# Kernel optimization log

Measured on AMD Instinct MI355X. Metric: run time of the kernel, lower is better.

The kernel has to match this reference:

```python
import jax, jax.numpy as jnp
import numpy as np

DIM = 128
KS = 7
HEADS = 4
HEAD_DIM = DIM // HEADS


def setup_inputs() -> dict:
    key = jax.random.key(0)
    ks = jax.random.split(key, 10)
    B, H, W, C = 4, 64, 64, DIM
    s = 0.02
    return {
        "x": jax.random.normal(ks[0], (B, H, W, C), jnp.float32),
        "qkv_w": jax.random.normal(ks[1], (C, 3 * C), jnp.float32) * s,
        "qkv_b": jnp.zeros((3 * C,), jnp.float32),
        "proj_w": jax.random.normal(ks[2], (C, C), jnp.float32) * s,
        "proj_b": jnp.zeros((C,), jnp.float32),
        "rpb": jax.random.normal(ks[3], (HEADS, 2 * KS - 1, 2 * KS - 1), jnp.float32) * s,
        "g1_w": jax.random.normal(ks[4], (C, C // 2), jnp.float32) * s,
        "g1_b": jnp.zeros((C // 2,), jnp.float32),
        "g2_w": jax.random.normal(ks[5], (C // 2, 1), jnp.float32) * s,
        "g2_b": jnp.zeros((1,), jnp.float32),
    }


def _neighborhood_attention(x, qkv_w, qkv_b, proj_w, proj_b, rpb):
    B, H, W, C = x.shape
    k = KS
    # qkv projection -> [B,H,W,3,heads,head_dim]
    qkv = (x @ qkv_w + qkv_b).reshape(B, H, W, 3, HEADS, HEAD_DIM)
    q = qkv[..., 0, :, :] * (HEAD_DIM ** -0.5)  # [B,H,W,h,d]
    kk = qkv[..., 1, :, :]
    v = qkv[..., 2, :, :]

    # Clamped sliding-window start indices (NATTEN semantics)
    sh = jnp.clip(jnp.arange(H) - k // 2, 0, H - k)  # [H]
    sw = jnp.clip(jnp.arange(W) - k // 2, 0, W - k)  # [W]
    idx_h = sh[:, None] + jnp.arange(k)[None, :]  # [H,k]
    idx_w = sw[:, None] + jnp.arange(k)[None, :]  # [W,k]

    # Gather neighborhood windows: [B,H,W,k,k,h,d]
    kwin = kk[:, idx_h[:, None, :, None], idx_w[None, :, None, :]]
    vwin = v[:, idx_h[:, None, :, None], idx_w[None, :, None, :]]

    # Relative position bias indices: (neighbor - query) + (k-1)
    bih = idx_h - jnp.arange(H)[:, None] + (k - 1)  # [H,k]
    biw = idx_w - jnp.arange(W)[:, None] + (k - 1)  # [W,k]
    # bias: [h,H,W,k,k] -> [H,W,h,k,k]
    bias = rpb[:, bih[:, None, :, None], biw[None, :, None, :]]
    bias = jnp.transpose(bias, (1, 2, 0, 3, 4))

    # scores: [B,H,W,h,k,k]
    scores = jnp.einsum('bxyhd,bxyklhd->bxyhkl', q, kwin) + bias[None]
    attn = jax.nn.softmax(scores.reshape(B, H, W, HEADS, k * k), axis=-1)
    attn = attn.reshape(B, H, W, HEADS, k, k)
    out = jnp.einsum('bxyhkl,bxyklhd->bxyhd', attn, vwin).reshape(B, H, W, C)
    return out @ proj_w + proj_b


def reference(x, qkv_w, qkv_b, proj_w, proj_b, rpb, g1_w, g1_b, g2_w, g2_b):
    attn_out = _neighborhood_attention(x, qkv_w, qkv_b, proj_w, proj_b, rpb)
    gate = jax.nn.sigmoid(jax.nn.relu(x @ g1_w + g1_b) @ g2_w + g2_b)  # [B,H,W,1]
    return attn_out * gate + x
```

## Files before the change

### kernel.cpp

```cpp
#include <hip/hip_runtime.h>
#include <hip/hip_bf16.h>
#include <math.h>

#define PIXELS 16384
#define C      128
#define KS     7
#define HEADS  4
#define HD     32
#define QSCALE 0.17677669529663687f

typedef __bf16 bf16x8 __attribute__((ext_vector_type(8)));
typedef __bf16 bf16x2 __attribute__((ext_vector_type(2)));
typedef float  f32x4  __attribute__((ext_vector_type(4)));
typedef float  f32x2  __attribute__((ext_vector_type(2)));

__device__ inline unsigned short f2bf(float f) {
    unsigned int u = __builtin_bit_cast(unsigned int, f);
    u += 0x7FFFu + ((u >> 16) & 1u);
    return (unsigned short)(u >> 16);
}
__device__ inline float bflo(unsigned int u) {
    return __builtin_bit_cast(float, u << 16);
}
__device__ inline float bfhi(unsigned int u) {
    return __builtin_bit_cast(float, u & 0xFFFF0000u);
}

__global__ __launch_bounds__(256) void prep_kernel(
    const float* __restrict__ qkv_w, const float* __restrict__ g1_w,
    const float* __restrict__ qkv_b, const float* __restrict__ g1_b,
    const float* __restrict__ proj_w,
    unsigned short* __restrict__ wT, unsigned short* __restrict__ pT,
    float* __restrict__ bias_ext)
{
    const int blk = blockIdx.x, tid = threadIdx.x;
    if (blk < 56) {
        int n = blk * 8 + (tid >> 5);
        int kq = tid & 31;
        float f0, f1, f2, f3;
        if (n < 384) {
            f0 = qkv_w[(kq*4+0)*384 + n]; f1 = qkv_w[(kq*4+1)*384 + n];
            f2 = qkv_w[(kq*4+2)*384 + n]; f3 = qkv_w[(kq*4+3)*384 + n];
        } else {
            int nn = n - 384;
            f0 = g1_w[(kq*4+0)*64 + nn]; f1 = g1_w[(kq*4+1)*64 + nn];
            f2 = g1_w[(kq*4+2)*64 + nn]; f3 = g1_w[(kq*4+3)*64 + nn];
        }
        ushort4 o; o.x = f2bf(f0); o.y = f2bf(f1); o.z = f2bf(f2); o.w = f2bf(f3);
        *(ushort4*)(wT + n*128 + kq*4) = o;
    } else if (blk < 72) {
        int n = (blk - 56) * 8 + (tid >> 5);
        int kq = tid & 31;
        ushort4 o;
        o.x = f2bf(proj_w[(kq*4+0)*128 + n]);
        o.y = f2bf(proj_w[(kq*4+1)*128 + n]);
        o.z = f2bf(proj_w[(kq*4+2)*128 + n]);
        o.w = f2bf(proj_w[(kq*4+3)*128 + n]);
        *(ushort4*)(pT + n*128 + kq*4) = o;
    } else {
        for (int idx = tid; idx < 448; idx += 256)
            bias_ext[idx] = (idx < 384) ? qkv_b[idx] : g1_b[idx - 384];
    }
}

__global__ __launch_bounds__(256) void gemm_qkvh_fused(
    const float* __restrict__ x, const unsigned short* __restrict__ wT,
    const float* __restrict__ bias_ext, const float* __restrict__ g2_w,
    const float* __restrict__ g2_b, unsigned short* __restrict__ qkvb,
    float* __restrict__ gate)
{
    __shared__ __align__(16) unsigned short As[64*128];
    __shared__ __align__(16) unsigned short Bs[64*128];
    __shared__ __align__(16) unsigned short Cs[64*64];
    const int grp = blockIdx.x;
    const int ntBeg = grp ? 4 : 0, ntEnd = grp ? 7 : 4;
    const int m0 = blockIdx.y * 64;
    const int tid = threadIdx.x;

#pragma unroll
    for (int it = 0; it < 4; it++) {
        int idx = tid + it*256, row = idx >> 4, c = idx & 15;
        const float* src = x + (size_t)(m0+row)*128 + c*8;
        float4 a = *(const float4*)src;
        float4 b2 = *(const float4*)(src + 4);
        uint4 v;
        v.x = (unsigned int)f2bf(a.x)  | ((unsigned int)f2bf(a.y)  << 16);
        v.y = (unsigned int)f2bf(a.z)  | ((unsigned int)f2bf(a.w)  << 16);
        v.z = (unsigned int)f2bf(b2.x) | ((unsigned int)f2bf(b2.y) << 16);
        v.w = (unsigned int)f2bf(b2.z) | ((unsigned int)f2bf(b2.w) << 16);
        *(uint4*)(As + row*128 + ((c ^ (row&7)) << 3)) = v;
    }

    const int wave = tid >> 6, lane = tid & 63;
    const int l15 = lane & 15, quad = lane >> 4;
    const int wm = (wave & 1) * 32, wn = (wave >> 1) * 32;

    for (int nt = ntBeg; nt < ntEnd; nt++) {
        const int n0 = nt * 64;
#pragma unroll
        for (int it = 0; it < 4; it++) {
            int idx = tid + it*256, row = idx >> 4, c = idx & 15;
            uint4 v = *(const uint4*)(wT + (size_t)(n0+row)*128 + c*8);
            *(uint4*)(Bs + row*128 + ((c ^ (row&7)) << 3)) = v;
        }
        __syncthreads();

        f32x4 acc[2][2] = {};
#pragma unroll
        for (int ks = 0; ks < 4; ks++) {
            bf16x8 af[2], bq[2];
#pragma unroll
            for (int mt = 0; mt < 2; mt++) {
                int m = wm + mt*16 + l15;
                af[mt] = *(const bf16x8*)(As + m*128 + (((ks*4+quad) ^ (m&7)) << 3));
            }
#pragma unroll
            for (int ntl = 0; ntl < 2; ntl++) {
                int n = wn + ntl*16 + l15;
                bq[ntl] = *(const bf16x8*)(Bs + n*128 + (((ks*4+quad) ^ (n&7)) << 3));
            }
#pragma unroll
            for (int mt = 0; mt < 2; mt++)
#pragma unroll
                for (int ntl = 0; ntl < 2; ntl++)
                    acc[mt][ntl] = __builtin_amdgcn_mfma_f32_16x16x32_bf16(
                        af[mt], bq[ntl], acc[mt][ntl], 0, 0, 0);
        }

        if (nt < 6) {
#pragma unroll
            for (int ntl = 0; ntl < 2; ntl++) {
                int nl = wn + ntl*16 + l15;
                int ng = n0 + nl;
                float qs = (ng < 128) ? QSCALE : 1.0f;
                float bv = bias_ext[ng];
#pragma unroll
                for (int mt = 0; mt < 2; mt++)
#pragma unroll
                    for (int r = 0; r < 4; r++) {
                        int ml = wm + mt*16 + quad*4 + r;
                        Cs[ml*64 + nl] = f2bf((acc[mt][ntl][r] + bv) * qs);
                    }
            }
            __syncthreads();
            int row = tid >> 2, part = tid & 3;
            uint4 a = *(const uint4*)(Cs + row*64 + part*16);
            uint4 b = *(const uint4*)(Cs + row*64 + part*16 + 8);
            unsigned short* dst = qkvb + (size_t)(m0+row)*384 + n0 + part*16;
            *(uint4*)dst = a;
            *(uint4*)(dst + 8) = b;
        } else {
            float* gpart = (float*)Cs;
            float rs[2][4];
#pragma unroll
            for (int mt = 0; mt < 2; mt++)
#pragma unroll
                for (int r = 0; r < 4; r++) rs[mt][r] = 0.0f;
#pragma unroll
            for (int ntl = 0; ntl < 2; ntl++) {
                int nl = wn + ntl*16 + l15;
                float bv = bias_ext[384 + nl];
                float gw = g2_w[nl];
#pragma unroll
                for (int mt = 0; mt < 2; mt++)
#pragma unroll
                    for (int r = 0; r < 4; r++) {
                        float h = acc[mt][ntl][r] + bv;
                        rs[mt][r] += fmaxf(h, 0.0f) * gw;
                    }
            }
#pragma unroll
            for (int off = 1; off <= 8; off <<= 1)
#pragma unroll
                for (int mt = 0; mt < 2; mt++)
#pragma unroll
                    for (int r = 0; r < 4; r++)
                        rs[mt][r] += __shfl_xor(rs[mt][r], off);
            if (l15 == 0) {
#pragma unroll
                for (int mt = 0; mt < 2; mt++)
#pragma unroll
                    for (int r = 0; r < 4; r++)
                        gpart[(wave >> 1)*64 + wm + mt*16 + quad*4 + r] = rs[mt][r];
            }
            __syncthreads();
            if (tid < 64) {
                float g = gpart[tid] + gpart[64 + tid] + g2_b[0];
                gate[m0 + tid] = 1.0f / (1.0f + __expf(-g));
            }
        }
    }
}

__global__ __launch_bounds__(128) void attn_kernel(
    const unsigned short* __restrict__ qkvb, const float* __restrict__ rpb,
    unsigned short* __restrict__ attnb)
{
    __shared__ __align__(16) unsigned short kvs[140 * 136];
    __shared__ float rpb_lds[2 * 169];

    const int blk = blockIdx.x;
    const int pr = blk & 1;
    const int tile = (blk >> 1) & 127;
    const int b = blk >> 8;
    const int ti0 = (tile >> 3) * 4, tj0 = (tile & 7) * 8;
    int wr0 = ti0 - 3; wr0 = wr0 < 0 ? 0 : (wr0 > 54 ? 54 : wr0);
    int wc0 = tj0 - 3; wc0 = wc0 < 0 ? 0 : (wc0 > 50 ? 50 : wc0);

    const int tid = threadIdx.x;
    const int hh = tid >> 6, lane = tid & 63;
    const int h = pr * 2 + hh;
    const int half = lane >> 5;
    const int p5 = lane & 31;
    const int pi = p5 >> 3, pj = p5 & 7;
    const int i = ti0 + pi, j = tj0 + pj;
    int sh = i - 3; sh = sh < 0 ? 0 : (sh > 57 ? 57 : sh);
    int sw = j - 3; sw = sw < 0 ? 0 : (sw > 57 ? 57 : sw);
    const int dr = sh - wr0, dc = sw - wc0;
    const size_t gp = (size_t)(((b << 6) + i) << 6) + j;

    unsigned int qu[8];
    const unsigned short* qptr = qkvb + gp * 384 + h * 32 + half * 16;
    *(uint4*)(qu + 0) = *(const uint4*)(qptr + 0);
    *(uint4*)(qu + 4) = *(const uint4*)(qptr + 8);

    float rpb_v[3];
#pragma unroll
    for (int t = 0; t < 3; t++) {
        int idx = tid + t * 128;
        rpb_v[t] = (idx < 338) ? rpb[pr * 338 + idx] : 0.0f;
    }

    for (int idx = tid; idx < 140 * 16; idx += 128) {
        int pos = idx >> 4, t = idx & 15;
        int wr = pos / 14, wc = pos - wr * 14;
        size_t gpos = (size_t)(((b << 6) + (wr0 + wr)) << 6) + (wc0 + wc);
        int src = 128 + ((t >> 3) << 7) + pr * 64 + ((t & 7) << 3);
        uint4 v = *(const uint4*)(qkvb + gpos * 384 + src);
        *(uint4*)(kvs + pos * 136 + ((t >> 3) << 6) + ((t & 7) << 3)) = v;
    }
#pragma unroll
    for (int t = 0; t < 3; t++) {
        int idx = tid + t * 128;
        if (idx < 338) rpb_lds[idx] = rpb_v[t];
    }
    __syncthreads();

    f32x2 acc2[8];
#pragma unroll
    for (int p = 0; p < 8; p++) acc2[p] = (f32x2){0.f, 0.f};
    float ssum = 0.0f;

    const float* rl = rpb_lds + hh * 169;
    const int rbase = (sh - i + 6) * 13 + (sw - j + 6);
    const int hwbase = (dr * 14 + dc) * 136 + hh * 32 + half * 16;

    for (int kr = 0; kr < 7; kr++) {
        const unsigned short* rowp = kvs + hwbase + kr * (14 * 136);
        const int ri = rbase + kr * 13;

        unsigned int ku[8], vu[8];
        *(uint4*)(ku + 0) = *(const uint4*)(rowp + 0);
        *(uint4*)(ku + 4) = *(const uint4*)(rowp + 8);
        *(uint4*)(vu + 0) = *(const uint4*)(rowp + 64);
        *(uint4*)(vu + 4) = *(const uint4*)(rowp + 72);

#pragma unroll
        for (int kc = 0; kc < 7; kc++) {
            unsigned int ku2[8], vu2[8];
            if (kc < 6) {
                const unsigned short* kpn = rowp + (kc + 1) * 136;
                *(uint4*)(ku2 + 0) = *(const uint4*)(kpn + 0);
                *(uint4*)(ku2 + 4) = *(const uint4*)(kpn + 8);
                *(uint4*)(vu2 + 0) = *(const uint4*)(kpn + 64);
                *(uint4*)(vu2 + 4) = *(const uint4*)(kpn + 72);
            }

            float s0 = 0.0f, s1 = 0.0f;
#if __has_builtin(__builtin_amdgcn_fdot2_f32_bf16)
#pragma unroll
            for (int p = 0; p < 4; p++) {
                s0 = __builtin_amdgcn_fdot2_f32_bf16(
                        __builtin_bit_cast(bf16x2, qu[p]),
                        __builtin_bit_cast(bf16x2, ku[p]), s0, false);
                s1 = __builtin_amdgcn_fdot2_f32_bf16(
                        __builtin_bit_cast(bf16x2, qu[p+4]),
                        __builtin_bit_cast(bf16x2, ku[p+4]), s1, false);
            }
#else
#pragma unroll
            for (int p = 0; p < 4; p++) {
                s0 += bflo(qu[p])   * bflo(ku[p])   + bfhi(qu[p])   * bfhi(ku[p]);
                s1 += bflo(qu[p+4]) * bflo(ku[p+4]) + bfhi(qu[p+4]) * bfhi(ku[p+4]);
            }
#endif
            float s = s0 + s1;
            s += __shfl_xor(s, 32);
            float e = __expf(s + rl[ri + kc]);
            ssum += e;

            f32x2 e2 = {e, e};
#pragma unroll
            for (int p = 0; p < 8; p++) {
                f32x2 v2 = {bflo(vu[p]), bfhi(vu[p])};
                acc2[p] += e2 * v2;
            }

            if (kc < 6) {
#pragma unroll
                for (int p = 0; p < 8; p++) { ku[p] = ku2[p]; vu[p] = vu2[p]; }
            }
        }
    }

    const float inv = 1.0f / ssum;
    unsigned int o[8];
#pragma unroll
    for (int p = 0; p < 8; p++) {
        unsigned int lo = f2bf(acc2[p].x * inv);
        unsigned int hi = f2bf(acc2[p].y * inv);
        o[p] = lo | (hi << 16);
    }
    unsigned short* op = attnb + gp * 128 + h * 32 + half * 16;
    *(uint4*)(op + 0) = *(const uint4*)(o + 0);
    *(uint4*)(op + 8) = *(const uint4*)(o + 4);
}

__global__ __launch_bounds__(256) void gemm_proj_mfma(
    const unsigned short* __restrict__ ab, const unsigned short* __restrict__ pT,
    const float* __restrict__ proj_b, const float* __restrict__ gate,
    const float* __restrict__ x, float* __restrict__ out)
{
    __shared__ __align__(16) unsigned short As[64*128];
    __shared__ __align__(16) unsigned short Bs[64*128];
    const int n0 = blockIdx.x * 64;
    const int m0 = blockIdx.y * 64;
    const int tid = threadIdx.x;

#pragma unroll
    for (int it = 0; it < 4; it++) {
        int idx = tid + it*256, row = idx >> 4, c = idx & 15;
        uint4 v = *(const uint4*)(ab + (size_t)(m0+row)*128 + c*8);
        *(uint4*)(As + row*128 + ((c ^ (row&7)) << 3)) = v;
    }
#pragma unroll
    for (int it = 0; it < 4; it++) {
        int idx = tid + it*256, row = idx >> 4, c = idx & 15;
        uint4 v = *(const uint4*)(pT + (size_t)(n0+row)*128 + c*8);
        *(uint4*)(Bs + row*128 + ((c ^ (row&7)) << 3)) = v;
    }
    __syncthreads();

    const int wave = tid >> 6, lane = tid & 63;
    const int l15 = lane & 15, quad = lane >> 4;
    const int wm = (wave & 1) * 32, wn = (wave >> 1) * 32;

    f32x4 acc[2][2] = {};
#pragma unroll
    for (int ks = 0; ks < 4; ks++) {
        bf16x8 af[2], bq[2];
#pragma unroll
        for (int mt = 0; mt < 2; mt++) {
            int m = wm + mt*16 + l15;
            af[mt] = *(const bf16x8*)(As + m*128 + (((ks*4+quad) ^ (m&7)) << 3));
        }
#pragma unroll
        for (int ntl = 0; ntl < 2; ntl++) {
            int n = wn + ntl*16 + l15;
            bq[ntl] = *(const bf16x8*)(Bs + n*128 + (((ks*4+quad) ^ (n&7)) << 3));
        }
#pragma unroll
        for (int mt = 0; mt < 2; mt++)
#pragma unroll
            for (int ntl = 0; ntl < 2; ntl++)
                acc[mt][ntl] = __builtin_amdgcn_mfma_f32_16x16x32_bf16(
                    af[mt], bq[ntl], acc[mt][ntl], 0, 0, 0);
    }
    __syncthreads();

    float* Cs = (float*)As;
#pragma unroll
    for (int ntl = 0; ntl < 2; ntl++) {
        int nl = wn + ntl*16 + l15;
        float bv = proj_b[n0 + nl];
#pragma unroll
        for (int mt = 0; mt < 2; mt++)
#pragma unroll
            for (int r = 0; r < 4; r++) {
                int ml = wm + mt*16 + quad*4 + r;
                Cs[ml*64 + nl] = acc[mt][ntl][r] + bv;
            }
    }
    __syncthreads();
    int row = tid >> 2, part = tid & 3;
    float gv = gate[m0 + row];
    const float* xr = x + (size_t)(m0+row)*128 + n0 + part*16;
    float* orow = out + (size_t)(m0+row)*128 + n0 + part*16;
#pragma unroll
    for (int q = 0; q < 4; q++) {
        float4 cv = *(const float4*)(Cs + row*64 + part*16 + q*4);
        float4 xv = *(const float4*)(xr + q*4);
        float4 o;
        o.x = cv.x * gv + xv.x; o.y = cv.y * gv + xv.y;
        o.z = cv.z * gv + xv.z; o.w = cv.w * gv + xv.w;
        *(float4*)(orow + q*4) = o;
    }
}

extern "C" void kernel_launch(void* const* d_in, const int* in_sizes, int n_in,
                              void* d_out, int out_size, void* d_ws, size_t ws_size,
                              hipStream_t stream)
{
    const float* x      = (const float*)d_in[0];
    const float* qkv_w  = (const float*)d_in[1];
    const float* qkv_b  = (const float*)d_in[2];
    const float* proj_w = (const float*)d_in[3];
    const float* proj_b = (const float*)d_in[4];
    const float* rpb    = (const float*)d_in[5];
    const float* g1_w   = (const float*)d_in[6];
    const float* g1_b   = (const float*)d_in[7];
    const float* g2_w   = (const float*)d_in[8];
    const float* g2_b   = (const float*)d_in[9];
    float* out = (float*)d_out;

    float* ws        = (float*)d_ws;
    float* gate      = ws;
    float* bias_ext  = gate + 16384;
    unsigned short* wT    = (unsigned short*)(bias_ext + 448);
    unsigned short* pT    = wT + 57344;
    unsigned short* qkvb  = pT + 16384;
    unsigned short* attnb = qkvb + 6291456;

    (void)in_sizes; (void)n_in; (void)out_size; (void)ws_size;

    prep_kernel<<<73, 256, 0, stream>>>(qkv_w, g1_w, qkv_b, g1_b, proj_w,
                                        wT, pT, bias_ext);
    gemm_qkvh_fused<<<dim3(2, 256), 256, 0, stream>>>(x, wT, bias_ext,
                                                      g2_w, g2_b, qkvb, gate);
    attn_kernel<<<1024, 128, 0, stream>>>(qkvb, rpb, attnb);
    gemm_proj_mfma<<<dim3(2, 256), 256, 0, stream>>>(attnb, pT, proj_b, gate, x, out);
}
```

Measured before the change: 115.4 us.

## Fuse all four kernels into one cooperative persistent kernel with grid syncs

Replaces the four separate launches (weight prep, QKV+gate GEMM, neighborhood attention, projection GEMM) with one cooperative kernel of 512 blocks that separates the stages with grid-wide syncs. The aim is to remove the launch gaps and per-kernel ramp-up and tail between stages. In exchange, each stage now runs with a fixed 512-block grid at 2 blocks per CU, set by the largest LDS footprint. Grid-sync barriers also add their own cost, and the old multi-kernel path is kept as a fallback if cooperative launch is unsupported.

```diff
diff --git a/kernel.cpp b/kernel.cpp
--- a/kernel.cpp
+++ b/kernel.cpp
@@ -1,6 +1,8 @@
 #include <hip/hip_runtime.h>
-#include <hip/hip_bf16.h>
+#include <hip/hip_cooperative_groups.h>
 #include <math.h>
+
+namespace cg = cooperative_groups;
 
 #define PIXELS 16384
 #define C      128
@@ -24,6 +26,394 @@
 }
 __device__ inline float bfhi(unsigned int u) {
     return __builtin_bit_cast(float, u & 0xFFFF0000u);
+}
+
+__global__ __launch_bounds__(256, 2) void fused_all(
+    const float* __restrict__ x,
+    const float* __restrict__ qkv_w, const float* __restrict__ qkv_b,
+    const float* __restrict__ proj_w, const float* __restrict__ proj_b,
+    const float* __restrict__ rpb,
+    const float* __restrict__ g1_w, const float* __restrict__ g1_b,
+    const float* __restrict__ g2_w, const float* __restrict__ g2_b,
+    float* __restrict__ out,
+    float* __restrict__ gate, float* __restrict__ bias_ext,
+    unsigned short* __restrict__ wT, unsigned short* __restrict__ pT,
+    unsigned short* __restrict__ qkvb, unsigned short* __restrict__ attnb)
+{
+    __shared__ alignas(16) unsigned char smem[196*136*2 + 338*4];
+    cg::grid_group grid = cg::this_grid();
+    const int bid = blockIdx.x;
+    const int tid = threadIdx.x;
+
+    if (bid < 73) {
+        const int blk = bid;
+        if (blk < 56) {
+            int n = blk * 8 + (tid >> 5);
+            int kq = tid & 31;
+            float f0, f1, f2, f3;
+            if (n < 384) {
+                f0 = qkv_w[(kq*4+0)*384 + n]; f1 = qkv_w[(kq*4+1)*384 + n];
+                f2 = qkv_w[(kq*4+2)*384 + n]; f3 = qkv_w[(kq*4+3)*384 + n];
+            } else {
+                int nn = n - 384;
+                f0 = g1_w[(kq*4+0)*64 + nn]; f1 = g1_w[(kq*4+1)*64 + nn];
+                f2 = g1_w[(kq*4+2)*64 + nn]; f3 = g1_w[(kq*4+3)*64 + nn];
+            }
+            ushort4 o; o.x = f2bf(f0); o.y = f2bf(f1); o.z = f2bf(f2); o.w = f2bf(f3);
+            *(ushort4*)(wT + n*128 + kq*4) = o;
+        } else if (blk < 72) {
+            int n = (blk - 56) * 8 + (tid >> 5);
+            int kq = tid & 31;
+            ushort4 o;
+            o.x = f2bf(proj_w[(kq*4+0)*128 + n]);
+            o.y = f2bf(proj_w[(kq*4+1)*128 + n]);
+            o.z = f2bf(proj_w[(kq*4+2)*128 + n]);
+            o.w = f2bf(proj_w[(kq*4+3)*128 + n]);
+            *(ushort4*)(pT + n*128 + kq*4) = o;
+        } else {
+            for (int idx = tid; idx < 448; idx += 256)
+                bias_ext[idx] = (idx < 384) ? qkv_b[idx] : g1_b[idx - 384];
+        }
+    }
+    __threadfence();
+    grid.sync();
+    __threadfence();
+
+    {
+        unsigned short* As = (unsigned short*)smem;
+        unsigned short* Bs = As + 64*128;
+        unsigned short* Cs = Bs + 64*128;
+        const int grp = bid >> 8;
+        const int ntBeg = grp ? 4 : 0, ntEnd = grp ? 7 : 4;
+        const int m0 = (bid & 255) * 64;
+
+#pragma unroll
+        for (int it = 0; it < 4; it++) {
+            int idx = tid + it*256, row = idx >> 4, c = idx & 15;
+            const float* src = x + (size_t)(m0+row)*128 + c*8;
+            float4 a = *(const float4*)src;
+            float4 b2 = *(const float4*)(src + 4);
+            uint4 v;
+            v.x = (unsigned int)f2bf(a.x)  | ((unsigned int)f2bf(a.y)  << 16);
+            v.y = (unsigned int)f2bf(a.z)  | ((unsigned int)f2bf(a.w)  << 16);
+            v.z = (unsigned int)f2bf(b2.x) | ((unsigned int)f2bf(b2.y) << 16);
+            v.w = (unsigned int)f2bf(b2.z) | ((unsigned int)f2bf(b2.w) << 16);
+            *(uint4*)(As + row*128 + ((c ^ (row&7)) << 3)) = v;
+        }
+
+        const int wave = tid >> 6, lane = tid & 63;
+        const int l15 = lane & 15, quad = lane >> 4;
+        const int wm = (wave & 1) * 32, wn = (wave >> 1) * 32;
+
+        for (int nt = ntBeg; nt < ntEnd; nt++) {
+            const int n0 = nt * 64;
+#pragma unroll
+            for (int it = 0; it < 4; it++) {
+                int idx = tid + it*256, row = idx >> 4, c = idx & 15;
+                uint4 v = *(const uint4*)(wT + (size_t)(n0+row)*128 + c*8);
+                *(uint4*)(Bs + row*128 + ((c ^ (row&7)) << 3)) = v;
+            }
+            __syncthreads();
+
+            f32x4 acc[2][2] = {};
+#pragma unroll
+            for (int ks = 0; ks < 4; ks++) {
+                bf16x8 af[2], bq[2];
+#pragma unroll
+                for (int mt = 0; mt < 2; mt++) {
+                    int m = wm + mt*16 + l15;
+                    af[mt] = *(const bf16x8*)(As + m*128 + (((ks*4+quad) ^ (m&7)) << 3));
+                }
+#pragma unroll
+                for (int ntl = 0; ntl < 2; ntl++) {
+                    int n = wn + ntl*16 + l15;
+                    bq[ntl] = *(const bf16x8*)(Bs + n*128 + (((ks*4+quad) ^ (n&7)) << 3));
+                }
+#pragma unroll
+                for (int mt = 0; mt < 2; mt++)
+#pragma unroll
+                    for (int ntl = 0; ntl < 2; ntl++)
+                        acc[mt][ntl] = __builtin_amdgcn_mfma_f32_16x16x32_bf16(
+                            af[mt], bq[ntl], acc[mt][ntl], 0, 0, 0);
+            }
+
+            if (nt < 6) {
+#pragma unroll
+                for (int ntl = 0; ntl < 2; ntl++) {
+                    int nl = wn + ntl*16 + l15;
+                    int ng = n0 + nl;
+                    float qs = (ng < 128) ? QSCALE : 1.0f;
+                    float bv = bias_ext[ng];
+#pragma unroll
+                    for (int mt = 0; mt < 2; mt++)
+#pragma unroll
+                        for (int r = 0; r < 4; r++) {
+                            int ml = wm + mt*16 + quad*4 + r;
+                            Cs[ml*64 + nl] = f2bf((acc[mt][ntl][r] + bv) * qs);
+                        }
+                }
+                __syncthreads();
+                int row = tid >> 2, part = tid & 3;
+                uint4 a = *(const uint4*)(Cs + row*64 + part*16);
+                uint4 b = *(const uint4*)(Cs + row*64 + part*16 + 8);
+                unsigned short* dst = qkvb + (size_t)(m0+row)*384 + n0 + part*16;
+                *(uint4*)dst = a;
+                *(uint4*)(dst + 8) = b;
+            } else {
+                float* gpart = (float*)Cs;
+                float rs[2][4];
+#pragma unroll
+                for (int mt = 0; mt < 2; mt++)
+#pragma unroll
+                    for (int r = 0; r < 4; r++) rs[mt][r] = 0.0f;
+#pragma unroll
+                for (int ntl = 0; ntl < 2; ntl++) {
+                    int nl = wn + ntl*16 + l15;
+                    float bv = bias_ext[384 + nl];
+                    float gw = g2_w[nl];
+#pragma unroll
+                    for (int mt = 0; mt < 2; mt++)
+#pragma unroll
+                        for (int r = 0; r < 4; r++) {
+                            float h = acc[mt][ntl][r] + bv;
+                            rs[mt][r] += fmaxf(h, 0.0f) * gw;
+                        }
+                }
+#pragma unroll
+                for (int off = 1; off <= 8; off <<= 1)
+#pragma unroll
+                    for (int mt = 0; mt < 2; mt++)
+#pragma unroll
+                        for (int r = 0; r < 4; r++)
+                            rs[mt][r] += __shfl_xor(rs[mt][r], off);
+                if (l15 == 0) {
+#pragma unroll
+                    for (int mt = 0; mt < 2; mt++)
+#pragma unroll
+                        for (int r = 0; r < 4; r++)
+                            gpart[(wave >> 1)*64 + wm + mt*16 + quad*4 + r] = rs[mt][r];
+                }
+                __syncthreads();
+                if (tid < 64) {
+                    float g = gpart[tid] + gpart[64 + tid] + g2_b[0];
+                    gate[m0 + tid] = 1.0f / (1.0f + __expf(-g));
+                }
+            }
+        }
+    }
+    __threadfence();
+    grid.sync();
+    __threadfence();
+
+    {
+        unsigned short* kvs = (unsigned short*)smem;
+        float* rpb_lds = (float*)(smem + 196*136*2);
+
+        const int pr = bid & 1;
+        const int tile = (bid >> 1) & 63;
+        const int b = bid >> 7;
+        const int ti0 = (tile >> 3) * 8, tj0 = (tile & 7) * 8;
+        int wr0 = ti0 - 3; wr0 = wr0 < 0 ? 0 : (wr0 > 50 ? 50 : wr0);
+        int wc0 = tj0 - 3; wc0 = wc0 < 0 ? 0 : (wc0 > 50 ? 50 : wc0);
+
+        const int hh = (tid >> 6) & 1;
+        const int pg = tid >> 7;
+        const int lane = tid & 63;
+        const int h = pr * 2 + hh;
+        const int half = lane >> 5;
+        const int p5 = lane & 31;
+        const int pi = pg * 4 + (p5 >> 3), pj = p5 & 7;
+        const int i = ti0 + pi, j = tj0 + pj;
+        int sh = i - 3; sh = sh < 0 ? 0 : (sh > 57 ? 57 : sh);
+        int sw = j - 3; sw = sw < 0 ? 0 : (sw > 57 ? 57 : sw);
+        const int dr = sh - wr0, dc = sw - wc0;
+        const size_t gp = (size_t)(((b << 6) + i) << 6) + j;
+
+        unsigned int qu[8];
+        const unsigned short* qptr = qkvb + gp * 384 + h * 32 + half * 16;
+        *(uint4*)(qu + 0) = *(const uint4*)(qptr + 0);
+        *(uint4*)(qu + 4) = *(const uint4*)(qptr + 8);
+
+        float rpb_v[2];
+#pragma unroll
+        for (int t = 0; t < 2; t++) {
+            int idx = tid + t * 256;
+            rpb_v[t] = (idx < 338) ? rpb[pr * 338 + idx] : 0.0f;
+        }
+
+        for (int idx = tid; idx < 196 * 16; idx += 256) {
+            int pos = idx >> 4, t = idx & 15;
+            int wr = pos / 14, wc = pos - wr * 14;
+            size_t gpos = (size_t)(((b << 6) + (wr0 + wr)) << 6) + (wc0 + wc);
+            int src = 128 + ((t >> 3) << 7) + pr * 64 + ((t & 7) << 3);
+            uint4 v = *(const uint4*)(qkvb + gpos * 384 + src);
+            *(uint4*)(kvs + pos * 136 + ((t >> 3) << 6) + ((t & 7) << 3)) = v;
+        }
+#pragma unroll
+        for (int t = 0; t < 2; t++) {
+            int idx = tid + t * 256;
+            if (idx < 338) rpb_lds[idx] = rpb_v[t];
+        }
+        __syncthreads();
+
+        f32x2 acc2[8];
+#pragma unroll
+        for (int p = 0; p < 8; p++) acc2[p] = (f32x2){0.f, 0.f};
+        float ssum = 0.0f;
+
+        const float* rl = rpb_lds + hh * 169;
+        const int rbase = (sh - i + 6) * 13 + (sw - j + 6);
+        const int hwbase = (dr * 14 + dc) * 136 + hh * 32 + half * 16;
+
+        for (int kr = 0; kr < 7; kr++) {
+            const unsigned short* rowp = kvs + hwbase + kr * (14 * 136);
+            const int ri = rbase + kr * 13;
+
+            unsigned int ku[8], vu[8];
+            *(uint4*)(ku + 0) = *(const uint4*)(rowp + 0);
+            *(uint4*)(ku + 4) = *(const uint4*)(rowp + 8);
+            *(uint4*)(vu + 0) = *(const uint4*)(rowp + 64);
+            *(uint4*)(vu + 4) = *(const uint4*)(rowp + 72);
+
+#pragma unroll
+            for (int kc = 0; kc < 7; kc++) {
+                unsigned int ku2[8], vu2[8];
+                if (kc < 6) {
+                    const unsigned short* kpn = rowp + (kc + 1) * 136;
+                    *(uint4*)(ku2 + 0) = *(const uint4*)(kpn + 0);
+                    *(uint4*)(ku2 + 4) = *(const uint4*)(kpn + 8);
+                    *(uint4*)(vu2 + 0) = *(const uint4*)(kpn + 64);
+                    *(uint4*)(vu2 + 4) = *(const uint4*)(kpn + 72);
+                }
+
+                float s0 = 0.0f, s1 = 0.0f;
+#if __has_builtin(__builtin_amdgcn_fdot2_f32_bf16)
+#pragma unroll
+                for (int p = 0; p < 4; p++) {
+                    s0 = __builtin_amdgcn_fdot2_f32_bf16(
+                            __builtin_bit_cast(bf16x2, qu[p]),
+                            __builtin_bit_cast(bf16x2, ku[p]), s0, false);
+                    s1 = __builtin_amdgcn_fdot2_f32_bf16(
+                            __builtin_bit_cast(bf16x2, qu[p+4]),
+                            __builtin_bit_cast(bf16x2, ku[p+4]), s1, false);
+                }
+#else
+#pragma unroll
+                for (int p = 0; p < 4; p++) {
+                    s0 += bflo(qu[p])   * bflo(ku[p])   + bfhi(qu[p])   * bfhi(ku[p]);
+                    s1 += bflo(qu[p+4]) * bflo(ku[p+4]) + bfhi(qu[p+4]) * bfhi(ku[p+4]);
+                }
+#endif
+                float s = s0 + s1;
+                s += __shfl_xor(s, 32);
+                float e = __expf(s + rl[ri + kc]);
+                ssum += e;
+
+                f32x2 e2 = {e, e};
+#pragma unroll
+                for (int p = 0; p < 8; p++) {
+                    f32x2 v2 = {bflo(vu[p]), bfhi(vu[p])};
+                    acc2[p] += e2 * v2;
+                }
+
+                if (kc < 6) {
+#pragma unroll
+                    for (int p = 0; p < 8; p++) { ku[p] = ku2[p]; vu[p] = vu2[p]; }
+                }
+            }
+        }
+
+        const float inv = 1.0f / ssum;
+        unsigned int o[8];
+#pragma unroll
+        for (int p = 0; p < 8; p++) {
+            unsigned int lo = f2bf(acc2[p].x * inv);
+            unsigned int hi = f2bf(acc2[p].y * inv);
+            o[p] = lo | (hi << 16);
+        }
+        unsigned short* op = attnb + gp * 128 + h * 32 + half * 16;
+        *(uint4*)(op + 0) = *(const uint4*)(o + 0);
+        *(uint4*)(op + 8) = *(const uint4*)(o + 4);
+    }
+    __threadfence();
+    grid.sync();
+    __threadfence();
+
+    {
+        unsigned short* As = (unsigned short*)smem;
+        unsigned short* Bs = As + 64*128;
+        const int n0 = (bid >> 8) * 64;
+        const int m0 = (bid & 255) * 64;
+
+#pragma unroll
+        for (int it = 0; it < 4; it++) {
+            int idx = tid + it*256, row = idx >> 4, c = idx & 15;
+            uint4 v = *(const uint4*)(attnb + (size_t)(m0+row)*128 + c*8);
+            *(uint4*)(As + row*128 + ((c ^ (row&7)) << 3)) = v;
+        }
+#pragma unroll
+        for (int it = 0; it < 4; it++) {
+            int idx = tid + it*256, row = idx >> 4, c = idx & 15;
+            uint4 v = *(const uint4*)(pT + (size_t)(n0+row)*128 + c*8);
+            *(uint4*)(Bs + row*128 + ((c ^ (row&7)) << 3)) = v;
+        }
+        __syncthreads();
+
+        const int wave = tid >> 6, lane = tid & 63;
+        const int l15 = lane & 15, quad = lane >> 4;
+        const int wm = (wave & 1) * 32, wn = (wave >> 1) * 32;
+
+        f32x4 acc[2][2] = {};
+#pragma unroll
+        for (int ks = 0; ks < 4; ks++) {
+            bf16x8 af[2], bq[2];
+#pragma unroll
+            for (int mt = 0; mt < 2; mt++) {
+                int m = wm + mt*16 + l15;
+                af[mt] = *(const bf16x8*)(As + m*128 + (((ks*4+quad) ^ (m&7)) << 3));
+            }
+#pragma unroll
+            for (int ntl = 0; ntl < 2; ntl++) {
+                int n = wn + ntl*16 + l15;
+                bq[ntl] = *(const bf16x8*)(Bs + n*128 + (((ks*4+quad) ^ (n&7)) << 3));
+            }
+#pragma unroll
+            for (int mt = 0; mt < 2; mt++)
+#pragma unroll
+                for (int ntl = 0; ntl < 2; ntl++)
+                    acc[mt][ntl] = __builtin_amdgcn_mfma_f32_16x16x32_bf16(
+                        af[mt], bq[ntl], acc[mt][ntl], 0, 0, 0);
+        }
+        __syncthreads();
+
+        float* Cs = (float*)As;
+#pragma unroll
+        for (int ntl = 0; ntl < 2; ntl++) {
+            int nl = wn + ntl*16 + l15;
+            float bv = proj_b[n0 + nl];
+#pragma unroll
+            for (int mt = 0; mt < 2; mt++)
+#pragma unroll
+                for (int r = 0; r < 4; r++) {
+                    int ml = wm + mt*16 + quad*4 + r;
+                    Cs[ml*64 + nl] = acc[mt][ntl][r] + bv;
+                }
+        }
+        __syncthreads();
+        int row = tid >> 2, part = tid & 3;
+        float gv = gate[m0 + row];
+        const float* xr = x + (size_t)(m0+row)*128 + n0 + part*16;
+        float* orow = out + (size_t)(m0+row)*128 + n0 + part*16;
+#pragma unroll
+        for (int q = 0; q < 4; q++) {
+            float4 cv = *(const float4*)(Cs + row*64 + part*16 + q*4);
+            float4 xv = *(const float4*)(xr + q*4);
+            float4 o;
+            o.x = cv.x * gv + xv.x; o.y = cv.y * gv + xv.y;
+            o.z = cv.z * gv + xv.z; o.w = cv.w * gv + xv.w;
+            *(float4*)(orow + q*4) = o;
+        }
+    }
 }
 
 __global__ __launch_bounds__(256) void prep_kernel(
@@ -433,6 +823,30 @@
 
     (void)in_sizes; (void)n_in; (void)out_size; (void)ws_size;
 
+    static int coop_ok = -1;
+    if (coop_ok < 0) {
+        int coop = 0, dev = 0;
+        (void)hipGetDevice(&dev);
+        (void)hipDeviceGetAttribute(&coop, hipDeviceAttributeCooperativeLaunch, dev);
+        int maxb = 0;
+        hipError_t oe = hipOccupancyMaxActiveBlocksPerMultiprocessor(
+            &maxb, fused_all, 256, 0);
+        coop_ok = (coop && oe == hipSuccess && maxb >= 2) ? 1 : 0;
+    }
+
+    if (coop_ok) {
+        void* args[] = { (void*)&x, (void*)&qkv_w, (void*)&qkv_b, (void*)&proj_w,
+                         (void*)&proj_b, (void*)&rpb, (void*)&g1_w, (void*)&g1_b,
+                         (void*)&g2_w, (void*)&g2_b, (void*)&out, (void*)&gate,
+                         (void*)&bias_ext, (void*)&wT, (void*)&pT, (void*)&qkvb,
+                         (void*)&attnb };
+        hipError_t le = hipLaunchCooperativeKernel((const void*)fused_all,
+                                                   dim3(512), dim3(256),
+                                                   args, 0, stream);
+        if (le == hipSuccess) return;
+        coop_ok = 0;
+    }
+
     prep_kernel<<<73, 256, 0, stream>>>(qkv_w, g1_w, qkv_b, g1_b, proj_w,
                                         wT, pT, bias_ext);
     gemm_qkvh_fused<<<dim3(2, 256), 256, 0, stream>>>(x, wT, bias_ext,
```

After: 115.9 us. No clear change (+0.4%).

## Fuse neighborhood attention with output projection and gated residual epilogue

Applied to the files above, without the earlier changes.

Adds a single attn_proj kernel in which each 512-thread block handles an 8x8 pixel tile across all four heads. The block loads a shared 14x14 K/V halo into LDS, computes attention with a register-prefetched softmax without max subtraction, and writes the bf16 result to swizzled LDS. It then runs the 128x128 projection GEMM with MFMA and applies the gate and residual before storing. This drops the attnb round trip through global memory and one kernel launch. The costs are large dynamic LDS (about 110 KB), only 256 blocks, which limits occupancy, and an extra host-side occupancy check with a fallback to the old two-kernel path.

```diff
diff --git a/kernel.cpp b/kernel.cpp
--- a/kernel.cpp
+++ b/kernel.cpp
@@ -1,5 +1,4 @@
 #include <hip/hip_runtime.h>
-#include <hip/hip_bf16.h>
 #include <math.h>
 
 #define PIXELS 16384
@@ -192,6 +191,218 @@
     }
 }
 
+#define ATTN_PROJ_LDS (196*264*2 + 676*4 + 64*128*2)
+
+__global__ __launch_bounds__(512) void attn_proj(
+    const unsigned short* __restrict__ qkvb, const float* __restrict__ rpb,
+    const unsigned short* __restrict__ pT, const float* __restrict__ proj_b,
+    const float* __restrict__ gate, const float* __restrict__ x,
+    float* __restrict__ out)
+{
+    extern __shared__ __align__(16) unsigned char dynsmem[];
+    unsigned short* kvs = (unsigned short*)dynsmem;
+    float* rpb_lds = (float*)(dynsmem + 196*264*2);
+    unsigned short* As = (unsigned short*)(dynsmem + 196*264*2 + 676*4);
+    unsigned short* Bs = (unsigned short*)dynsmem;
+    float* Cs = (float*)(dynsmem + 32768);
+
+    const int bid = blockIdx.x;
+    const int b = bid >> 6;
+    const int tile = bid & 63;
+    const int ti0 = (tile >> 3) * 8, tj0 = (tile & 7) * 8;
+    int wr0 = ti0 - 3; wr0 = wr0 < 0 ? 0 : (wr0 > 50 ? 50 : wr0);
+    int wc0 = tj0 - 3; wc0 = wc0 < 0 ? 0 : (wc0 > 50 ? 50 : wc0);
+
+    const int tid = threadIdx.x;
+    const int wave = tid >> 6, lane = tid & 63;
+    const int h = wave & 3;
+    const int pg = wave >> 2;
+    const int half = lane >> 5;
+    const int p5 = lane & 31;
+    const int pi = pg * 4 + (p5 >> 3), pj = p5 & 7;
+    const int i = ti0 + pi, j = tj0 + pj;
+    int sh = i - 3; sh = sh < 0 ? 0 : (sh > 57 ? 57 : sh);
+    int sw = j - 3; sw = sw < 0 ? 0 : (sw > 57 ? 57 : sw);
+    const int dr = sh - wr0, dc = sw - wc0;
+    const size_t gp = (size_t)(((b << 6) + i) << 6) + j;
+
+    unsigned int qu[8];
+    const unsigned short* qptr = qkvb + gp * 384 + h * 32 + half * 16;
+    *(uint4*)(qu + 0) = *(const uint4*)(qptr + 0);
+    *(uint4*)(qu + 4) = *(const uint4*)(qptr + 8);
+
+    float rpb_v[2];
+#pragma unroll
+    for (int t = 0; t < 2; t++) {
+        int idx = tid + t * 512;
+        rpb_v[t] = (idx < 676) ? rpb[idx] : 0.0f;
+    }
+
+    for (int idx = tid; idx < 196 * 32; idx += 512) {
+        int pos = idx >> 5, t = idx & 31;
+        int wr = pos / 14, wc = pos - wr * 14;
+        size_t gpos = (size_t)(((b << 6) + (wr0 + wr)) << 6) + (wc0 + wc);
+        uint4 v = *(const uint4*)(qkvb + gpos * 384 + 128 + t * 8);
+        *(uint4*)(kvs + pos * 264 + t * 8) = v;
+    }
+#pragma unroll
+    for (int t = 0; t < 2; t++) {
+        int idx = tid + t * 512;
+        if (idx < 676) rpb_lds[idx] = rpb_v[t];
+    }
+    __syncthreads();
+
+    f32x2 acc2[8];
+#pragma unroll
+    for (int p = 0; p < 8; p++) acc2[p] = (f32x2){0.f, 0.f};
+    float ssum = 0.0f;
+
+    const float* rl = rpb_lds + h * 169;
+    const int rbase = (sh - i + 6) * 13 + (sw - j + 6);
+    const int hwbase = (dr * 14 + dc) * 264 + h * 32 + half * 16;
+
+    for (int kr = 0; kr < 7; kr++) {
+        const unsigned short* rowp = kvs + hwbase + kr * (14 * 264);
+        const int ri = rbase + kr * 13;
+
+        unsigned int ku[8], vu[8];
+        *(uint4*)(ku + 0) = *(const uint4*)(rowp + 0);
+        *(uint4*)(ku + 4) = *(const uint4*)(rowp + 8);
+        *(uint4*)(vu + 0) = *(const uint4*)(rowp + 128);
+        *(uint4*)(vu + 4) = *(const uint4*)(rowp + 136);
+
+#pragma unroll
+        for (int kc = 0; kc < 7; kc++) {
+            unsigned int ku2[8], vu2[8];
+            if (kc < 6) {
+                const unsigned short* kpn = rowp + (kc + 1) * 264;
+                *(uint4*)(ku2 + 0) = *(const uint4*)(kpn + 0);
+                *(uint4*)(ku2 + 4) = *(const uint4*)(kpn + 8);
+                *(uint4*)(vu2 + 0) = *(const uint4*)(kpn + 128);
+                *(uint4*)(vu2 + 4) = *(const uint4*)(kpn + 136);
+            }
+
+            float s0 = 0.0f, s1 = 0.0f;
+#if __has_builtin(__builtin_amdgcn_fdot2_f32_bf16)
+#pragma unroll
+            for (int p = 0; p < 4; p++) {
+                s0 = __builtin_amdgcn_fdot2_f32_bf16(
+                        __builtin_bit_cast(bf16x2, qu[p]),
+                        __builtin_bit_cast(bf16x2, ku[p]), s0, false);
+                s1 = __builtin_amdgcn_fdot2_f32_bf16(
+                        __builtin_bit_cast(bf16x2, qu[p+4]),
+                        __builtin_bit_cast(bf16x2, ku[p+4]), s1, false);
+            }
+#else
+#pragma unroll
+            for (int p = 0; p < 4; p++) {
+                s0 += bflo(qu[p])   * bflo(ku[p])   + bfhi(qu[p])   * bfhi(ku[p]);
+                s1 += bflo(qu[p+4]) * bflo(ku[p+4]) + bfhi(qu[p+4]) * bfhi(ku[p+4]);
+            }
+#endif
+            float s = s0 + s1;
+            s += __shfl_xor(s, 32);
+            float e = __expf(s + rl[ri + kc]);
+            ssum += e;
+
+            f32x2 e2 = {e, e};
+#pragma unroll
+            for (int p = 0; p < 8; p++) {
+                f32x2 v2 = {bflo(vu[p]), bfhi(vu[p])};
+                acc2[p] += e2 * v2;
+            }
+
+            if (kc < 6) {
+#pragma unroll
+                for (int p = 0; p < 8; p++) { ku[p] = ku2[p]; vu[p] = vu2[p]; }
+            }
+        }
+    }
+
+    {
+        const float inv = 1.0f / ssum;
+        unsigned int o[8];
+#pragma unroll
+        for (int p = 0; p < 8; p++) {
+            unsigned int lo = f2bf(acc2[p].x * inv);
+            unsigned int hi = f2bf(acc2[p].y * inv);
+            o[p] = lo | (hi << 16);
+        }
+        const int pix = pi * 8 + pj;
+        const int c0 = h * 4 + half * 2;
+        *(uint4*)(As + pix*128 + (((c0  ) ^ (pix&7)) << 3)) = *(const uint4*)(o + 0);
+        *(uint4*)(As + pix*128 + (((c0+1) ^ (pix&7)) << 3)) = *(const uint4*)(o + 4);
+    }
+    __syncthreads();
+
+#pragma unroll
+    for (int it = 0; it < 4; it++) {
+        int idx = tid + it*512, row = idx >> 4, c = idx & 15;
+        uint4 v = *(const uint4*)(pT + (size_t)row*128 + c*8);
+        *(uint4*)(Bs + row*128 + ((c ^ (row&7)) << 3)) = v;
+    }
+    __syncthreads();
+
+    {
+        const int l15 = lane & 15, quad = lane >> 4;
+        const int wm = (wave & 1) * 32, wn = (wave >> 1) * 32;
+
+        f32x4 acc[2][2] = {};
+#pragma unroll
+        for (int ks = 0; ks < 4; ks++) {
+            bf16x8 af[2], bq[2];
+#pragma unroll
+            for (int mt = 0; mt < 2; mt++) {
+                int m = wm + mt*16 + l15;
+                af[mt] = *(const bf16x8*)(As + m*128 + (((ks*4+quad) ^ (m&7)) << 3));
+            }
+#pragma unroll
+            for (int ntl = 0; ntl < 2; ntl++) {
+                int n = wn + ntl*16 + l15;
+                bq[ntl] = *(const bf16x8*)(Bs + n*128 + (((ks*4+quad) ^ (n&7)) << 3));
+            }
+#pragma unroll
+            for (int mt = 0; mt < 2; mt++)
+#pragma unroll
+                for (int ntl = 0; ntl < 2; ntl++)
+                    acc[mt][ntl] = __builtin_amdgcn_mfma_f32_16x16x32_bf16(
+                        af[mt], bq[ntl], acc[mt][ntl], 0, 0, 0);
+        }
+
+#pragma unroll
+        for (int ntl = 0; ntl < 2; ntl++) {
+            int nl = wn + ntl*16 + l15;
+            float bv = proj_b[nl];
+#pragma unroll
+            for (int mt = 0; mt < 2; mt++)
+#pragma unroll
+                for (int r = 0; r < 4; r++) {
+                    int ml = wm + mt*16 + quad*4 + r;
+                    Cs[ml*128 + nl] = acc[mt][ntl][r] + bv;
+                }
+        }
+    }
+    __syncthreads();
+
+    {
+        int pix = tid >> 3, part = tid & 7;
+        int gi = ti0 + (pix >> 3), gj = tj0 + (pix & 7);
+        size_t gr = (size_t)(((b << 6) + gi) << 6) + gj;
+        float gv = gate[gr];
+        const float* xr = x + gr*128 + part*16;
+        float* orow = out + gr*128 + part*16;
+#pragma unroll
+        for (int q = 0; q < 4; q++) {
+            float4 cv = *(const float4*)(Cs + pix*128 + part*16 + q*4);
+            float4 xv = *(const float4*)(xr + q*4);
+            float4 o;
+            o.x = cv.x * gv + xv.x; o.y = cv.y * gv + xv.y;
+            o.z = cv.z * gv + xv.z; o.w = cv.w * gv + xv.w;
+            *(float4*)(orow + q*4) = o;
+        }
+    }
+}
+
 __global__ __launch_bounds__(128) void attn_kernel(
     const unsigned short* __restrict__ qkvb, const float* __restrict__ rpb,
     unsigned short* __restrict__ attnb)
@@ -433,10 +644,27 @@
 
     (void)in_sizes; (void)n_in; (void)out_size; (void)ws_size;
 
+    static int fused_ok = -1;
+    if (fused_ok < 0) {
+        hipError_t ae = hipFuncSetAttribute(
+            (const void*)attn_proj,
+            hipFuncAttributeMaxDynamicSharedMemorySize, ATTN_PROJ_LDS);
+        int maxb = 0;
+        hipError_t oe = hipOccupancyMaxActiveBlocksPerMultiprocessor(
+            &maxb, attn_proj, 512, ATTN_PROJ_LDS);
+        fused_ok = (ae == hipSuccess && oe == hipSuccess && maxb >= 1) ? 1 : 0;
+    }
+
     prep_kernel<<<73, 256, 0, stream>>>(qkv_w, g1_w, qkv_b, g1_b, proj_w,
                                         wT, pT, bias_ext);
     gemm_qkvh_fused<<<dim3(2, 256), 256, 0, stream>>>(x, wT, bias_ext,
                                                       g2_w, g2_b, qkvb, gate);
-    attn_kernel<<<1024, 128, 0, stream>>>(qkvb, rpb, attnb);
-    gemm_proj_mfma<<<dim3(2, 256), 256, 0, stream>>>(attnb, pT, proj_b, gate, x, out);
-}
+    if (fused_ok) {
+        attn_proj<<<256, 512, ATTN_PROJ_LDS, stream>>>(qkvb, rpb, pT, proj_b,
+                                                       gate, x, out);
+    } else {
+        attn_kernel<<<1024, 128, 0, stream>>>(qkvb, rpb, attnb);
+        gemm_proj_mfma<<<dim3(2, 256), 256, 0, stream>>>(attnb, pT, proj_b,
+                                                         gate, x, out);
+    }
+}
```

Result: faster. 111.4 us (-3.5%).
